# Kernel optimization log

Hardware: AMD Instinct MI355X
Metric: run time of the kernel (lower is better)

The kernel has to match this reference:

```python
import jax, jax.numpy as jnp
import numpy as np

CH = 256
IC = 128  # inter_channels = channels // reduction
TEMP = 0.05


def setup_inputs() -> dict:
    key = jax.random.key(0)
    k1, k2, k3, k4, k5 = jax.random.split(key, 5)
    x = jax.random.normal(k1, (8, CH, 64, 64), dtype=jnp.float32)
    # 1x1 conv weights stored as [out_ch, in_ch]
    w_qkv = jax.random.normal(k2, (3 * IC, CH), dtype=jnp.float32) * 0.01
    b_qkv = jax.random.normal(k3, (3 * IC,), dtype=jnp.float32) * 0.01
    w_out = jax.random.normal(k4, (CH, IC), dtype=jnp.float32) * 0.01
    b_out = jax.random.normal(k5, (CH,), dtype=jnp.float32) * 0.01
    return {"x": x, "w_qkv": w_qkv, "b_qkv": b_qkv, "w_out": w_out, "b_out": b_out}


def reference(x, w_qkv, b_qkv, w_out, b_out):
    b, c, h, w = x.shape
    n = h * w
    ic = w_qkv.shape[0] // 3
    # 1x1 conv QKV projection
    qkv = jnp.einsum('bchw,oc->bohw', x, w_qkv) + b_qkv[None, :, None, None]
    qkv = qkv.reshape(b, 3, ic, n)
    q, k, v = qkv[:, 0], qkv[:, 1], qkv[:, 2]  # each [b, ic, n]
    # mean-center q and k over spatial positions (per channel)
    k = k - k.mean(axis=-1, keepdims=True)
    q = q - q.mean(axis=-1, keepdims=True)
    # pairwise_weight[b, i, j] = sum_c k[b, c, i] * q[b, c, j]
    pw = jnp.einsum('bci,bcj->bij', k, q)
    pw = pw / jnp.sqrt(jnp.float32(ic))  # use_scale=True
    pw = pw / TEMP
    pw = jax.nn.softmax(pw, axis=-1)  # [b, n, n]
    # y[b, c, i] = sum_j pw[b, i, j] * v[b, c, j]
    y = jnp.einsum('bij,bcj->bci', pw, v).reshape(b, ic, h, w)
    out = x + jnp.einsum('bchw,oc->bohw', y, w_out) + b_out[None, :, None, None]
    return out
```

## Files before the change

### kernel.cpp

```cpp
#include <hip/hip_runtime.h>
#include <hip/hip_bf16.h>

typedef __bf16 bf16_t;
typedef __bf16 bf16x4 __attribute__((ext_vector_type(4)));
typedef __bf16 bf16x8 __attribute__((ext_vector_type(8)));
typedef float f32x4 __attribute__((ext_vector_type(4)));

#define MFMA16(a, b, c) __builtin_amdgcn_mfma_f32_16x16x32_bf16((a), (b), (c), 0, 0, 0)

constexpr int BATCH = 8, CH = 256, IC = 128, NPOS = 4096;
constexpr float SM_C = 2.5503488f;

constexpr size_t OFF_XT    = 0;
constexpr size_t OFF_QT    = 16777216;
constexpr size_t OFF_KT    = 25165824;
constexpr size_t OFF_V     = 33554432;
constexpr size_t OFF_WQKV  = 41943040;
constexpr size_t OFF_WOUT  = 42139648;
constexpr size_t OFF_XMEAN = 42205184;
constexpr size_t OFF_QKM   = 42213376;
constexpr size_t OFF_PL    = 42221568;

__device__ __forceinline__ void gload_lds16(const char* g, char* lds) {
    __builtin_amdgcn_global_load_lds((const __attribute__((address_space(1))) unsigned int*)g,
                                     (__attribute__((address_space(3))) unsigned int*)lds, 16, 0,
                                     0);
}

__global__ void k_convert_w(const float* __restrict__ wqkv, const float* __restrict__ wout,
                            bf16_t* __restrict__ wqkv_b, bf16_t* __restrict__ wout_b) {
    int idx = blockIdx.x * 256 + threadIdx.x;
    if (idx < 384 * 256) wqkv_b[idx] = (bf16_t)wqkv[idx];
    int j = idx - 384 * 256;
    if (j >= 0 && j < 256 * 128) wout_b[j] = (bf16_t)wout[j];
}

__global__ void k_xmean(const float* __restrict__ x, float* __restrict__ xmean) {
    int c = blockIdx.x, b = blockIdx.y;
    const float4* xv = (const float4*)(x + ((size_t)(b * CH + c)) * NPOS);
    float s = 0.f;
#pragma unroll
    for (int r = 0; r < 4; r++) {
        float4 v = xv[r * 256 + threadIdx.x];
        s += v.x + v.y + v.z + v.w;
    }
    __shared__ float red[256];
    red[threadIdx.x] = s;
    __syncthreads();
    for (int st = 128; st > 0; st >>= 1) {
        if (threadIdx.x < st) red[threadIdx.x] += red[threadIdx.x + st];
        __syncthreads();
    }
    if (threadIdx.x == 0) xmean[b * CH + c] = red[0] * (1.0f / NPOS);
}

__global__ void k_qkmean(const float* __restrict__ wqkv, const float* __restrict__ xmean,
                         float* __restrict__ qkm) {
    int o = blockIdx.x, b = blockIdx.y, lane = threadIdx.x;
    float4 w = ((const float4*)(wqkv + (size_t)o * CH))[lane];
    float4 xm = ((const float4*)(xmean + b * CH))[lane];
    float s = w.x * xm.x + w.y * xm.y + w.z * xm.z + w.w * xm.w;
#pragma unroll
    for (int m = 1; m < 64; m <<= 1) s += __shfl_xor(s, m, 64);
    if (lane == 0) qkm[b * CH + o] = s;
}

__global__ void k_transpose(const float* __restrict__ x, bf16_t* __restrict__ xt) {
    __shared__ float t[32][33];
    int p0 = blockIdx.x * 32, c0 = blockIdx.y * 32, b = blockIdx.z;
    int i = threadIdx.x >> 5, j = threadIdx.x & 31;
#pragma unroll
    for (int q = 0; q < 4; q++) {
        int c = c0 + q * 8 + i;
        t[q * 8 + i][j] = x[((size_t)(b * CH + c)) * NPOS + p0 + j];
    }
    __syncthreads();
#pragma unroll
    for (int q = 0; q < 4; q++) {
        int p = p0 + q * 8 + i;
        xt[((size_t)(b * NPOS + p)) * CH + c0 + j] = (bf16_t)t[j][q * 8 + i];
    }
}

__global__ __launch_bounds__(256, 2) void k_qkv(const bf16_t* __restrict__ xt,
                                                const bf16_t* __restrict__ wqkv_b,
                                                const float* __restrict__ qkm,
                                                const float* __restrict__ b_qkv,
                                                bf16_t* __restrict__ qt, bf16_t* __restrict__ kt,
                                                bf16_t* __restrict__ v) {
    int bid = blockIdx.x;
    int b = bid & 7;
    int r0 = bid >> 3;
    int sec = r0 % 3;
    int pt = r0 / 3;
    int p0 = pt * 128;
    int wid = threadIdx.x >> 6, lane = threadIdx.x & 63;
    int g = lane >> 4, li = lane & 15;
    int wr = wid >> 1, wc = wid & 1;
    f32x4 acc[4][4] = {};
    if (sec < 2) {
        int ob = sec * 128;
#pragma unroll 1
        for (int kk = 0; kk < 8; kk++) {
            bf16x8 af[4], bfg[4];
#pragma unroll
            for (int fa = 0; fa < 4; fa++) {
                int p = p0 + wr * 64 + fa * 16 + li;
                af[fa] = *(const bf16x8*)(xt + ((size_t)(b * NPOS + p)) * CH + kk * 32 + g * 8);
            }
#pragma unroll
            for (int fb = 0; fb < 4; fb++) {
                int o = ob + wc * 64 + fb * 16 + li;
                bfg[fb] = *(const bf16x8*)(wqkv_b + (size_t)o * CH + kk * 32 + g * 8);
            }
#pragma unroll
            for (int fa = 0; fa < 4; fa++)
#pragma unroll
                for (int fb = 0; fb < 4; fb++) acc[fa][fb] = MFMA16(af[fa], bfg[fb], acc[fa][fb]);
        }
        bf16_t* dst = (sec == 0) ? qt : kt;
#pragma unroll
        for (int fb = 0; fb < 4; fb++) {
            int ol = wc * 64 + fb * 16 + li;
            float mean = qkm[b * CH + sec * 128 + ol];
#pragma unroll
            for (int fa = 0; fa < 4; fa++)
#pragma unroll
                for (int r = 0; r < 4; r++) {
                    int p = p0 + wr * 64 + fa * 16 + g * 4 + r;
                    dst[((size_t)(b * NPOS + p)) * IC + ol] = (bf16_t)(acc[fa][fb][r] - mean);
                }
        }
    } else {
#pragma unroll 1
        for (int kk = 0; kk < 8; kk++) {
            bf16x8 af[4], bfg[4];
#pragma unroll
            for (int fa = 0; fa < 4; fa++) {
                int o = 256 + wr * 64 + fa * 16 + li;
                af[fa] = *(const bf16x8*)(wqkv_b + (size_t)o * CH + kk * 32 + g * 8);
            }
#pragma unroll
            for (int fb = 0; fb < 4; fb++) {
                int p = p0 + wc * 64 + fb * 16 + li;
                bfg[fb] = *(const bf16x8*)(xt + ((size_t)(b * NPOS + p)) * CH + kk * 32 + g * 8);
            }
#pragma unroll
            for (int fa = 0; fa < 4; fa++)
#pragma unroll
                for (int fb = 0; fb < 4; fb++) acc[fa][fb] = MFMA16(af[fa], bfg[fb], acc[fa][fb]);
        }
#pragma unroll
        for (int fa = 0; fa < 4; fa++)
#pragma unroll
            for (int r = 0; r < 4; r++) {
                int oe = wr * 64 + fa * 16 + g * 4 + r;
                float bias = b_qkv[256 + oe];
#pragma unroll
                for (int fb = 0; fb < 4; fb++) {
                    int p = p0 + wc * 64 + fb * 16 + li;
                    v[((size_t)(b * IC + oe)) * NPOS + p] = (bf16_t)(acc[fa][fb][r] + bias);
                }
            }
    }
}

constexpr int TJ = 64;

__global__ __launch_bounds__(256, 2) void k_attn(const bf16_t* __restrict__ qt,
                                                 const bf16_t* __restrict__ kt,
                                                 const bf16_t* __restrict__ v,
                                                 bf16_t* __restrict__ pacc,
                                                 float* __restrict__ pl) {
    __shared__ __attribute__((aligned(128))) char smem[2 * 32768 + 4 * 32 * 128];
    const int bid = blockIdx.x;
    const int b = bid & 7;
    const int r0 = bid >> 3;
    const int jh = r0 & 1;
    const int it = r0 >> 1;
    const int jbase = jh * 2048;
    const int wid = threadIdx.x >> 6, lane = threadIdx.x & 63;
    const int g = lane >> 4, li = lane & 15;
    const int iw0 = it * 128 + wid * 32;
    const bf16_t* ktb = kt + (size_t)b * NPOS * IC;
    const bf16_t* qtb = qt + (size_t)b * NPOS * IC;
    const bf16_t* vb = v + (size_t)b * IC * NPOS;
    char* pw = smem + 65536 + wid * 4096;

    int qoff_[4], voff_[4];
#pragma unroll
    for (int u = 0; u < 4; u++) {
        int t = wid * 4 + u;
        int qrow = 4 * t + (lane >> 4);
        qoff_[u] = qrow * 256 + (((lane & 15) ^ (qrow & 7)) << 4);
        int vrow = 8 * t + (lane >> 3);
        voff_[u] = vrow * 8192 + (((lane & 7) ^ (vrow & 7)) << 4);
    }

    auto stage = [&](int dstpar, int sj) {
        const char* qs = (const char*)qtb + (size_t)sj * 256;
        const char* vs = (const char*)vb + (size_t)sj * 2;
        char* qd = smem + dstpar * 32768;
        char* vd = qd + 16384;
#pragma unroll
        for (int u = 0; u < 4; u++) {
            gload_lds16(qs + qoff_[u], qd + (wid * 4 + u) * 1024);
            gload_lds16(vs + voff_[u], vd + (wid * 4 + u) * 1024);
        }
    };

    stage(0, jbase);

    bf16x8 a[2][4];
#pragma unroll
    for (int fi = 0; fi < 2; fi++)
#pragma unroll
        for (int kk = 0; kk < 4; kk++)
            a[fi][kk] = *(const bf16x8*)(ktb + (size_t)(iw0 + fi * 16 + li) * IC + kk * 32 + g * 8);

    f32x4 acc[2][8] = {};
    float lsum[2] = {0.f, 0.f};

    auto body = [&](int par, int nextj) {
        stage(par ^ 1, nextj);
        asm volatile("s_waitcnt vmcnt(8)" ::: "memory");
        __builtin_amdgcn_s_barrier();
        asm volatile("" ::: "memory");
        const char* qb = smem + par * 32768;
        const char* vbuf = qb + 16384;
        f32x4 s[2][4] = {};
#pragma unroll
        for (int jf = 0; jf < 4; jf++) {
            bf16x8 bq[4];
#pragma unroll
            for (int kk = 0; kk < 4; kk++)
                bq[kk] = *(const bf16x8*)(qb + (jf * 16 + li) * 256 +
                                          (((kk * 4 + g) ^ (li & 7)) << 4));
#pragma unroll
            for (int fi = 0; fi < 2; fi++)
#pragma unroll
                for (int kk = 0; kk < 4; kk++) s[fi][jf] = MFMA16(bq[kk], a[fi][kk], s[fi][jf]);
        }
#pragma unroll
        for (int fi = 0; fi < 2; fi++) {
            int row = fi * 16 + li;
#pragma unroll
            for (int jf = 0; jf < 4; jf++) {
                float p0 = exp2f(s[fi][jf][0] * SM_C);
                float p1 = exp2f(s[fi][jf][1] * SM_C);
                float p2 = exp2f(s[fi][jf][2] * SM_C);
                float p3 = exp2f(s[fi][jf][3] * SM_C);
                lsum[fi] += (p0 + p1) + (p2 + p3);
                bf16x4 pk = {(bf16_t)p0, (bf16_t)p1, (bf16_t)p2, (bf16_t)p3};
                *(bf16x4*)(pw + row * 128 + ((((jf * 2 + (g >> 1)) ^ (row & 7))) << 4) +
                           ((g & 1) << 3)) = pk;
            }
        }
#pragma unroll
        for (int jj = 0; jj < 2; jj++) {
            bf16x8 pf[2];
#pragma unroll
            for (int fi = 0; fi < 2; fi++) {
                int row = fi * 16 + li;
                pf[fi] = *(const bf16x8*)(pw + row * 128 + (((jj * 4 + g) ^ (row & 7)) << 4));
            }
#pragma unroll
            for (int cf = 0; cf < 8; cf++) {
                bf16x8 vf = *(const bf16x8*)(vbuf + (cf * 16 + li) * 128 +
                                             (((jj * 4 + g) ^ (li & 7)) << 4));
#pragma unroll
                for (int fi = 0; fi < 2; fi++) acc[fi][cf] = MFMA16(pf[fi], vf, acc[fi][cf]);
            }
        }
        asm volatile("" ::: "memory");
        __builtin_amdgcn_s_barrier();
    };

#pragma unroll 1
    for (int jo = 0; jo < 2048; jo += 2 * TJ) {
        body(0, jbase + ((jo + TJ) & 2047));
        body(1, jbase + ((jo + 2 * TJ) & 2047));
    }

#pragma unroll
    for (int fi = 0; fi < 2; fi++) {
        lsum[fi] += __shfl_xor(lsum[fi], 16, 64);
        lsum[fi] += __shfl_xor(lsum[fi], 32, 64);
    }
    if (g == 0) {
#pragma unroll
        for (int fi = 0; fi < 2; fi++)
            pl[((size_t)(b * 2 + jh)) * NPOS + iw0 + fi * 16 + li] = lsum[fi];
    }
    bf16_t* po = pacc + ((size_t)(b * 2 + jh)) * NPOS * IC;
#pragma unroll
    for (int fi = 0; fi < 2; fi++)
#pragma unroll
        for (int r = 0; r < 4; r++) {
            int i = iw0 + fi * 16 + g * 4 + r;
#pragma unroll
            for (int cf = 0; cf < 8; cf++)
                po[(size_t)i * IC + cf * 16 + li] = (bf16_t)acc[fi][cf][r];
        }
}

__global__ void k_merge(const bf16_t* __restrict__ pacc, const float* __restrict__ pl,
                        bf16_t* __restrict__ yt) {
    int idx = blockIdx.x * 256 + threadIdx.x;
    int co = idx & 15;
    int i = (idx >> 4) & 4095;
    int b = idx >> 16;
    const bf16x8* p0 = (const bf16x8*)pacc + ((size_t)(b * 2 + 0) * NPOS + i) * 16 + co;
    const bf16x8* p1 = (const bf16x8*)pacc + ((size_t)(b * 2 + 1) * NPOS + i) * 16 + co;
    float l = pl[(size_t)(b * 2 + 0) * NPOS + i] + pl[(size_t)(b * 2 + 1) * NPOS + i];
    float inv = 1.0f / l;
    bf16x8 a0 = *p0, a1 = *p1, o;
#pragma unroll
    for (int j = 0; j < 8; j++) o[j] = (bf16_t)(((float)a0[j] + (float)a1[j]) * inv);
    *((bf16x8*)yt + ((size_t)b * NPOS + i) * 16 + co) = o;
}

__global__ __launch_bounds__(256, 2) void k_out(const bf16_t* __restrict__ yt,
                                                const bf16_t* __restrict__ wout_b,
                                                const float* __restrict__ x,
                                                const float* __restrict__ b_out,
                                                float* __restrict__ out) {
    int bid = blockIdx.x;
    int b = bid & 7;
    int r0 = bid >> 3;
    int oct = r0 & 1, pt = r0 >> 1;
    int p0 = pt * 128, oc0 = oct * 128;
    int wid = threadIdx.x >> 6, lane = threadIdx.x & 63;
    int g = lane >> 4, li = lane & 15;
    int wr = wid >> 1, wc = wid & 1;
    f32x4 acc[4][4] = {};
#pragma unroll
    for (int kk = 0; kk < 4; kk++) {
        bf16x8 af[4], bfg[4];
#pragma unroll
        for (int fa = 0; fa < 4; fa++) {
            int oc = oc0 + wr * 64 + fa * 16 + li;
            af[fa] = *(const bf16x8*)(wout_b + (size_t)oc * IC + kk * 32 + g * 8);
        }
#pragma unroll
        for (int fb = 0; fb < 4; fb++) {
            int p = p0 + wc * 64 + fb * 16 + li;
            bfg[fb] = *(const bf16x8*)(yt + ((size_t)(b * NPOS + p)) * IC + kk * 32 + g * 8);
        }
#pragma unroll
        for (int fa = 0; fa < 4; fa++)
#pragma unroll
            for (int fb = 0; fb < 4; fb++) acc[fa][fb] = MFMA16(af[fa], bfg[fb], acc[fa][fb]);
    }
#pragma unroll
    for (int fa = 0; fa < 4; fa++)
#pragma unroll
        for (int r = 0; r < 4; r++) {
            int oc = oc0 + wr * 64 + fa * 16 + g * 4 + r;
            float bias = b_out[oc];
#pragma unroll
            for (int fb = 0; fb < 4; fb++) {
                int p = p0 + wc * 64 + fb * 16 + li;
                size_t idx = ((size_t)(b * CH + oc)) * NPOS + p;
                out[idx] = acc[fa][fb][r] + x[idx] + bias;
            }
        }
}

extern "C" void kernel_launch(void* const* d_in, const int* in_sizes, int n_in, void* d_out,
                              int out_size, void* d_ws, size_t ws_size, hipStream_t stream) {
    const float* x = (const float*)d_in[0];
    const float* w_qkv = (const float*)d_in[1];
    const float* b_qkv = (const float*)d_in[2];
    const float* w_out = (const float*)d_in[3];
    const float* b_out = (const float*)d_in[4];
    float* out = (float*)d_out;
    char* ws = (char*)d_ws;

    bf16_t* xt = (bf16_t*)(ws + OFF_XT);
    bf16_t* pacc = (bf16_t*)(ws + OFF_XT);
    bf16_t* qt = (bf16_t*)(ws + OFF_QT);
    bf16_t* kt = (bf16_t*)(ws + OFF_KT);
    bf16_t* yt = (bf16_t*)(ws + OFF_KT);
    bf16_t* v = (bf16_t*)(ws + OFF_V);
    bf16_t* wqkv_b = (bf16_t*)(ws + OFF_WQKV);
    bf16_t* wout_b = (bf16_t*)(ws + OFF_WOUT);
    float* xmean = (float*)(ws + OFF_XMEAN);
    float* qkm = (float*)(ws + OFF_QKM);
    float* pl = (float*)(ws + OFF_PL);

    k_convert_w<<<512, 256, 0, stream>>>(w_qkv, w_out, wqkv_b, wout_b);
    k_xmean<<<dim3(256, 8), 256, 0, stream>>>(x, xmean);
    k_qkmean<<<dim3(256, 8), 64, 0, stream>>>(w_qkv, xmean, qkm);
    k_transpose<<<dim3(128, 8, 8), 256, 0, stream>>>(x, xt);
    k_qkv<<<768, 256, 0, stream>>>(xt, wqkv_b, qkm, b_qkv, qt, kt, v);
    k_attn<<<512, 256, 0, stream>>>(qt, kt, v, pacc, pl);
    k_merge<<<2048, 256, 0, stream>>>(pacc, pl, yt);
    k_out<<<512, 256, 0, stream>>>(yt, wout_b, x, b_out, out);
}
```

Before: 163.3 us.

## Switch attention to 32x32 MFMA with register-resident P via permlane swap

Rewrites the attention inner loop to use 32x32x16 bf16 MFMA, computing S transposed so the exponentiated probabilities can be repacked in registers with v_permlane32_swap instead of round-tripping through LDS. The softmax scale is folded into K during the projection kernel, and raw v_exp_f32 and packed bf16 conversion instructions replace exp2f and scalar casts. This removes the per-wave LDS P buffer and its write/read traffic and cuts MFMA issue count, at the cost of relying on gfx950-specific instructions and more register pressure from 16-wide accumulators.

```diff
diff --git a/kernel.cpp b/kernel.cpp
--- a/kernel.cpp
+++ b/kernel.cpp
@@ -2,11 +2,12 @@
 #include <hip/hip_bf16.h>
 
 typedef __bf16 bf16_t;
-typedef __bf16 bf16x4 __attribute__((ext_vector_type(4)));
 typedef __bf16 bf16x8 __attribute__((ext_vector_type(8)));
 typedef float f32x4 __attribute__((ext_vector_type(4)));
+typedef float f32x16 __attribute__((ext_vector_type(16)));
 
 #define MFMA16(a, b, c) __builtin_amdgcn_mfma_f32_16x16x32_bf16((a), (b), (c), 0, 0, 0)
+#define MFMA32(a, b, c) __builtin_amdgcn_mfma_f32_32x32x16_bf16((a), (b), (c), 0, 0, 0)
 
 constexpr int BATCH = 8, CH = 256, IC = 128, NPOS = 4096;
 constexpr float SM_C = 2.5503488f;
@@ -25,6 +26,16 @@
     __builtin_amdgcn_global_load_lds((const __attribute__((address_space(1))) unsigned int*)g,
                                      (__attribute__((address_space(3))) unsigned int*)lds, 16, 0,
                                      0);
+}
+__device__ __forceinline__ float fexp2(float x) {
+    float r;
+    asm("v_exp_f32 %0, %1" : "=v"(r) : "v"(x));
+    return r;
+}
+__device__ __forceinline__ int cvtpk(float lo, float hi) {
+    int r;
+    asm("v_cvt_pk_bf16_f32 %0, %1, %2" : "=v"(r) : "v"(lo), "v"(hi));
+    return r;
 }
 
 __global__ void k_convert_w(const float* __restrict__ wqkv, const float* __restrict__ wout,
@@ -119,6 +130,7 @@
                 for (int fb = 0; fb < 4; fb++) acc[fa][fb] = MFMA16(af[fa], bfg[fb], acc[fa][fb]);
         }
         bf16_t* dst = (sec == 0) ? qt : kt;
+        float scale = (sec == 1) ? SM_C : 1.0f;
 #pragma unroll
         for (int fb = 0; fb < 4; fb++) {
             int ol = wc * 64 + fb * 16 + li;
@@ -128,7 +140,8 @@
 #pragma unroll
                 for (int r = 0; r < 4; r++) {
                     int p = p0 + wr * 64 + fa * 16 + g * 4 + r;
-                    dst[((size_t)(b * NPOS + p)) * IC + ol] = (bf16_t)(acc[fa][fb][r] - mean);
+                    dst[((size_t)(b * NPOS + p)) * IC + ol] =
+                        (bf16_t)((acc[fa][fb][r] - mean) * scale);
                 }
         }
     } else {
@@ -172,7 +185,7 @@
                                                  const bf16_t* __restrict__ v,
                                                  bf16_t* __restrict__ pacc,
                                                  float* __restrict__ pl) {
-    __shared__ __attribute__((aligned(128))) char smem[2 * 32768 + 4 * 32 * 128];
+    __shared__ __attribute__((aligned(128))) char smem[2 * 32768];
     const int bid = blockIdx.x;
     const int b = bid & 7;
     const int r0 = bid >> 3;
@@ -180,12 +193,11 @@
     const int it = r0 >> 1;
     const int jbase = jh * 2048;
     const int wid = threadIdx.x >> 6, lane = threadIdx.x & 63;
-    const int g = lane >> 4, li = lane & 15;
+    const int col = lane & 31, h = lane >> 5;
     const int iw0 = it * 128 + wid * 32;
     const bf16_t* ktb = kt + (size_t)b * NPOS * IC;
     const bf16_t* qtb = qt + (size_t)b * NPOS * IC;
     const bf16_t* vb = v + (size_t)b * IC * NPOS;
-    char* pw = smem + 65536 + wid * 4096;
 
     int qoff_[4], voff_[4];
 #pragma unroll
@@ -211,15 +223,13 @@
 
     stage(0, jbase);
 
-    bf16x8 a[2][4];
-#pragma unroll
-    for (int fi = 0; fi < 2; fi++)
-#pragma unroll
-        for (int kk = 0; kk < 4; kk++)
-            a[fi][kk] = *(const bf16x8*)(ktb + (size_t)(iw0 + fi * 16 + li) * IC + kk * 32 + g * 8);
-
-    f32x4 acc[2][8] = {};
-    float lsum[2] = {0.f, 0.f};
+    bf16x8 bk[8];
+#pragma unroll
+    for (int ks = 0; ks < 8; ks++)
+        bk[ks] = *(const bf16x8*)(ktb + (size_t)(iw0 + col) * IC + ks * 16 + h * 8);
+
+    f32x16 acc[4] = {};
+    float ls[4] = {0.f, 0.f, 0.f, 0.f};
 
     auto body = [&](int par, int nextj) {
         stage(par ^ 1, nextj);
@@ -228,48 +238,43 @@
         asm volatile("" ::: "memory");
         const char* qb = smem + par * 32768;
         const char* vbuf = qb + 16384;
-        f32x4 s[2][4] = {};
-#pragma unroll
-        for (int jf = 0; jf < 4; jf++) {
-            bf16x8 bq[4];
-#pragma unroll
-            for (int kk = 0; kk < 4; kk++)
-                bq[kk] = *(const bf16x8*)(qb + (jf * 16 + li) * 256 +
-                                          (((kk * 4 + g) ^ (li & 7)) << 4));
-#pragma unroll
-            for (int fi = 0; fi < 2; fi++)
-#pragma unroll
-                for (int kk = 0; kk < 4; kk++) s[fi][jf] = MFMA16(bq[kk], a[fi][kk], s[fi][jf]);
-        }
-#pragma unroll
-        for (int fi = 0; fi < 2; fi++) {
-            int row = fi * 16 + li;
-#pragma unroll
-            for (int jf = 0; jf < 4; jf++) {
-                float p0 = exp2f(s[fi][jf][0] * SM_C);
-                float p1 = exp2f(s[fi][jf][1] * SM_C);
-                float p2 = exp2f(s[fi][jf][2] * SM_C);
-                float p3 = exp2f(s[fi][jf][3] * SM_C);
-                lsum[fi] += (p0 + p1) + (p2 + p3);
-                bf16x4 pk = {(bf16_t)p0, (bf16_t)p1, (bf16_t)p2, (bf16_t)p3};
-                *(bf16x4*)(pw + row * 128 + ((((jf * 2 + (g >> 1)) ^ (row & 7))) << 4) +
-                           ((g & 1) << 3)) = pk;
-            }
-        }
-#pragma unroll
-        for (int jj = 0; jj < 2; jj++) {
-            bf16x8 pf[2];
-#pragma unroll
-            for (int fi = 0; fi < 2; fi++) {
-                int row = fi * 16 + li;
-                pf[fi] = *(const bf16x8*)(pw + row * 128 + (((jj * 4 + g) ^ (row & 7)) << 4));
-            }
-#pragma unroll
-            for (int cf = 0; cf < 8; cf++) {
-                bf16x8 vf = *(const bf16x8*)(vbuf + (cf * 16 + li) * 128 +
-                                             (((jj * 4 + g) ^ (li & 7)) << 4));
-#pragma unroll
-                for (int fi = 0; fi < 2; fi++) acc[fi][cf] = MFMA16(pf[fi], vf, acc[fi][cf]);
+#pragma unroll
+        for (int jsub = 0; jsub < 2; jsub++) {
+            f32x16 s = {};
+#pragma unroll
+            for (int ks = 0; ks < 8; ks++) {
+                bf16x8 aq = *(const bf16x8*)(qb + (jsub * 32 + col) * 256 +
+                                             (((ks * 2 + h) ^ (col & 7)) << 4));
+                s = MFMA32(aq, bk[ks], s);
+            }
+            float e[16];
+#pragma unroll
+            for (int r = 0; r < 16; r++) e[r] = fexp2(s[r]);
+#pragma unroll
+            for (int r = 0; r < 16; r++) ls[r & 3] += e[r];
+            int w[8];
+#pragma unroll
+            for (int q = 0; q < 8; q++) w[q] = cvtpk(e[2 * q], e[2 * q + 1]);
+            asm("v_permlane32_swap_b32 %0, %1" : "+v"(w[0]), "+v"(w[2]));
+            asm("v_permlane32_swap_b32 %0, %1" : "+v"(w[1]), "+v"(w[3]));
+            asm("v_permlane32_swap_b32 %0, %1" : "+v"(w[4]), "+v"(w[6]));
+            asm("v_permlane32_swap_b32 %0, %1" : "+v"(w[5]), "+v"(w[7]));
+            union {
+                int u[4];
+                bf16x8 v;
+            } pb0, pb1;
+            pb0.u[0] = w[0]; pb0.u[1] = w[1]; pb0.u[2] = w[2]; pb0.u[3] = w[3];
+            pb1.u[0] = w[4]; pb1.u[1] = w[5]; pb1.u[2] = w[6]; pb1.u[3] = w[7];
+#pragma unroll
+            for (int kl = 0; kl < 2; kl++) {
+                int kg = jsub * 2 + kl;
+                bf16x8 pbf = kl == 0 ? pb0.v : pb1.v;
+#pragma unroll
+                for (int cs = 0; cs < 4; cs++) {
+                    bf16x8 av = *(const bf16x8*)(vbuf + (cs * 32 + col) * 128 +
+                                                 (((kg * 2 + h) ^ (col & 7)) << 4));
+                    acc[cs] = MFMA32(av, pbf, acc[cs]);
+                }
             }
         }
         asm volatile("" ::: "memory");
@@ -282,25 +287,19 @@
         body(1, jbase + ((jo + 2 * TJ) & 2047));
     }
 
-#pragma unroll
-    for (int fi = 0; fi < 2; fi++) {
-        lsum[fi] += __shfl_xor(lsum[fi], 16, 64);
-        lsum[fi] += __shfl_xor(lsum[fi], 32, 64);
-    }
-    if (g == 0) {
-#pragma unroll
-        for (int fi = 0; fi < 2; fi++)
-            pl[((size_t)(b * 2 + jh)) * NPOS + iw0 + fi * 16 + li] = lsum[fi];
-    }
+    float lsum = (ls[0] + ls[1]) + (ls[2] + ls[3]);
+    lsum += __shfl_xor(lsum, 32, 64);
+    const int i = iw0 + col;
+    if (h == 0) pl[((size_t)(b * 2 + jh)) * NPOS + i] = lsum;
+
     bf16_t* po = pacc + ((size_t)(b * 2 + jh)) * NPOS * IC;
 #pragma unroll
-    for (int fi = 0; fi < 2; fi++)
-#pragma unroll
-        for (int r = 0; r < 4; r++) {
-            int i = iw0 + fi * 16 + g * 4 + r;
-#pragma unroll
-            for (int cf = 0; cf < 8; cf++)
-                po[(size_t)i * IC + cf * 16 + li] = (bf16_t)acc[fi][cf][r];
+    for (int cs = 0; cs < 4; cs++)
+#pragma unroll
+        for (int q = 0; q < 8; q++) {
+            int u = cvtpk(acc[cs][2 * q], acc[cs][2 * q + 1]);
+            int c0 = cs * 32 + ((q & 1) << 1) + ((q >> 1) << 3) + 4 * h;
+            *(int*)((char*)po + ((size_t)i * IC + c0) * 2) = u;
         }
 }
 
```

Result: faster. 149.2 us (-8.7%).
